# Kernel tuning notes

Measured on AMD Instinct MI355X. Metric: run time of the kernel, lower is better.

Reference implementation:

```python
import jax, jax.numpy as jnp
import numpy as np


def setup_inputs() -> dict:
    key = jax.random.key(0)
    k1, k2, k3, k4 = jax.random.split(key, 4)
    B, N, F, H, C = 16, 4096, 8, 64, 256
    x = jax.random.normal(k1, (B, N, F, H), dtype=jnp.float32)
    W = jax.random.normal(k2, (H, 1), dtype=jnp.float32) / jnp.sqrt(jnp.float32(H))
    b = jax.random.normal(k3, (1,), dtype=jnp.float32) * 0.01
    segment_ids = jax.random.randint(k4, (N,), 0, C)
    return {"x": x, "W": W, "b": b, "segment_ids": segment_ids, "num_coarse": C}


def reference(x, W, b, segment_ids, num_coarse):
    # x: [B, N, F, H]; segment_ids: [N] -> coarse index; output: [B, C, F, H]
    B, N, Fdim, H = x.shape
    seg = segment_ids
    # node scores: Linear(hidden_dim, 1) on mean over feature axis -> [B, N]
    scores = (jnp.einsum('bnfh,ho->bn', x, W) / jnp.float32(Fdim)) + b[0]
    # numerically-stable per-segment softmax over fine nodes within each coarse group
    seg_max = jax.vmap(lambda s: jax.ops.segment_max(s, seg, num_segments=num_coarse))(scores)  # [B, C]
    e = jnp.exp(scores - seg_max[:, seg])                                                        # [B, N]
    denom = jax.vmap(lambda ee: jax.ops.segment_sum(ee, seg, num_segments=num_coarse))(e)        # [B, C]
    w = e / denom[:, seg]                                                                        # [B, N]
    # score-weighted segmented sum of fine features into coarse nodes
    pooled = jax.vmap(
        lambda wb, xb: jax.ops.segment_sum(wb[:, None, None] * xb, seg, num_segments=num_coarse)
    )(w, x)  # [B, C, F, H]
    return pooled
```

## Files before the change

### kernel.cpp

```cpp
#include <hip/hip_runtime.h>

#define B_ 16
#define N_ 4096
#define F_ 8
#define H_ 64
#define C_ 256
#define FH 512
#define CAP 256

__global__ __launch_bounds__(128) void fused_pool_kernel(
    const float* __restrict__ x, const float* __restrict__ W,
    const float* __restrict__ bias, const int* __restrict__ seg,
    float* __restrict__ out)
{
    int b    = blockIdx.x >> 8;
    int c    = blockIdx.x & (C_ - 1);
    int t    = threadIdx.x;
    int wave = t >> 6;
    int lane = t & 63;

    __shared__ int   list[CAP];
    __shared__ int   cnt;
    __shared__ float combine[FH];
    __shared__ float esum_s;

    if (t == 0) cnt = 0;
    __syncthreads();

    const int4* seg4 = (const int4*)seg;
#pragma unroll
    for (int k = 0; k < N_ / (128 * 4); k++) {
        int i4 = t + k * 128;
        int4 s4 = seg4[i4];
        int n0 = i4 * 4;
        if (s4.x == c) { int p = atomicAdd(&cnt, 1); if (p < CAP) list[p] = n0; }
        if (s4.y == c) { int p = atomicAdd(&cnt, 1); if (p < CAP) list[p] = n0 + 1; }
        if (s4.z == c) { int p = atomicAdd(&cnt, 1); if (p < CAP) list[p] = n0 + 2; }
        if (s4.w == c) { int p = atomicAdd(&cnt, 1); if (p < CAP) list[p] = n0 + 3; }
    }
    __syncthreads();
    int m = cnt;
    if (m > CAP) m = CAP;

    float4 w4 = *(const float4*)(W + ((4 * lane) & 63));
    float  bb = bias[0];

    const float4* x4 = (const float4*)x;
    float4 acc0 = {0, 0, 0, 0}, acc1 = {0, 0, 0, 0};
    float  esum = 0.0f;

    for (int i = wave; i < m; i += 2) {
        int n = list[i];
        size_t rb = ((size_t)(b * N_ + n)) * (FH / 4);
        float4 v0 = x4[rb + lane];
        float4 v1 = x4[rb + 64 + lane];
        float p = (v0.x + v1.x) * w4.x + (v0.y + v1.y) * w4.y
                + (v0.z + v1.z) * w4.z + (v0.w + v1.w) * w4.w;
#pragma unroll
        for (int off = 32; off > 0; off >>= 1)
            p += __shfl_xor(p, off, 64);
        float e = __expf(p * (1.0f / F_) + bb);
        esum += e;
        acc0.x += e * v0.x; acc0.y += e * v0.y; acc0.z += e * v0.z; acc0.w += e * v0.w;
        acc1.x += e * v1.x; acc1.y += e * v1.y; acc1.z += e * v1.z; acc1.w += e * v1.w;
    }

    if (wave == 0) {
        *(float4*)&combine[4 * lane]       = acc0;
        *(float4*)&combine[4 * lane + 256] = acc1;
        if (lane == 0) esum_s = esum;
    }
    __syncthreads();
    if (wave == 1) {
        float4 o0 = *(float4*)&combine[4 * lane];
        float4 o1 = *(float4*)&combine[4 * lane + 256];
        float denom = esum + esum_s;
        float inv = (m > 0) ? 1.0f / denom : 0.0f;
        float4 r0, r1;
        r0.x = (acc0.x + o0.x) * inv; r0.y = (acc0.y + o0.y) * inv;
        r0.z = (acc0.z + o0.z) * inv; r0.w = (acc0.w + o0.w) * inv;
        r1.x = (acc1.x + o1.x) * inv; r1.y = (acc1.y + o1.y) * inv;
        r1.z = (acc1.z + o1.z) * inv; r1.w = (acc1.w + o1.w) * inv;
        size_t ob = ((size_t)(b * C_ + c)) * (FH / 4);
        ((float4*)out)[ob + lane]      = r0;
        ((float4*)out)[ob + 64 + lane] = r1;
    }
}

extern "C" void kernel_launch(void* const* d_in, const int* in_sizes, int n_in,
                              void* d_out, int out_size, void* d_ws, size_t ws_size,
                              hipStream_t stream)
{
    const float* x    = (const float*)d_in[0];
    const float* W    = (const float*)d_in[1];
    const float* bias = (const float*)d_in[2];
    const int*   seg  = (const int*)d_in[3];
    float* out = (float*)d_out;

    fused_pool_kernel<<<B_ * C_, 128, 0, stream>>>(x, W, bias, seg, out);
}
```

Measured before the change: 210.4 us.

## Assign one wave per batch, share segment list across four batches per block

Each block now handles one coarse segment for four batches, one wave per batch, so the segment-id scan and list build are amortized over four batches instead of being repeated per batch. Each wave walks the full member list itself and unrolls by two rows for more memory-level parallelism, which removes the cross-wave LDS combine and its barrier. In exchange there are four times fewer blocks and longer serial loops per wave, and register use per thread goes up.

```diff
diff --git a/kernel.cpp b/kernel.cpp
--- a/kernel.cpp
+++ b/kernel.cpp
@@ -8,29 +8,27 @@
 #define FH 512
 #define CAP 256
 
-__global__ __launch_bounds__(128) void fused_pool_kernel(
+__global__ __launch_bounds__(256) void fused_pool_kernel(
     const float* __restrict__ x, const float* __restrict__ W,
     const float* __restrict__ bias, const int* __restrict__ seg,
     float* __restrict__ out)
 {
-    int b    = blockIdx.x >> 8;
     int c    = blockIdx.x & (C_ - 1);
+    int g    = blockIdx.x >> 8;
     int t    = threadIdx.x;
     int wave = t >> 6;
     int lane = t & 63;
+    int b    = g * 4 + wave;
 
-    __shared__ int   list[CAP];
-    __shared__ int   cnt;
-    __shared__ float combine[FH];
-    __shared__ float esum_s;
-
+    __shared__ int list[CAP];
+    __shared__ int cnt;
     if (t == 0) cnt = 0;
     __syncthreads();
 
     const int4* seg4 = (const int4*)seg;
 #pragma unroll
-    for (int k = 0; k < N_ / (128 * 4); k++) {
-        int i4 = t + k * 128;
+    for (int k = 0; k < N_ / (256 * 4); k++) {
+        int i4 = t + k * 256;
         int4 s4 = seg4[i4];
         int n0 = i4 * 4;
         if (s4.x == c) { int p = atomicAdd(&cnt, 1); if (p < CAP) list[p] = n0; }
@@ -46,45 +44,64 @@
     float  bb = bias[0];
 
     const float4* x4 = (const float4*)x;
-    float4 acc0 = {0, 0, 0, 0}, acc1 = {0, 0, 0, 0};
+    size_t batch_base = (size_t)b * N_ * (FH / 4);
+
+    float4 accA0 = {0, 0, 0, 0}, accA1 = {0, 0, 0, 0};
+    float4 accB0 = {0, 0, 0, 0}, accB1 = {0, 0, 0, 0};
     float  esum = 0.0f;
 
-    for (int i = wave; i < m; i += 2) {
-        int n = list[i];
-        size_t rb = ((size_t)(b * N_ + n)) * (FH / 4);
-        float4 v0 = x4[rb + lane];
-        float4 v1 = x4[rb + 64 + lane];
-        float p = (v0.x + v1.x) * w4.x + (v0.y + v1.y) * w4.y
-                + (v0.z + v1.z) * w4.z + (v0.w + v1.w) * w4.w;
+    int i = 0;
+    for (; i + 2 <= m; i += 2) {
+        int na = list[i], nb = list[i + 1];
+        size_t ra = batch_base + (size_t)na * (FH / 4);
+        size_t rb = batch_base + (size_t)nb * (FH / 4);
+        float4 a0 = x4[ra + lane];
+        float4 a1 = x4[ra + 64 + lane];
+        float4 b0 = x4[rb + lane];
+        float4 b1 = x4[rb + 64 + lane];
+
+        float pa = (a0.x + a1.x) * w4.x + (a0.y + a1.y) * w4.y
+                 + (a0.z + a1.z) * w4.z + (a0.w + a1.w) * w4.w;
+        float pb = (b0.x + b1.x) * w4.x + (b0.y + b1.y) * w4.y
+                 + (b0.z + b1.z) * w4.z + (b0.w + b1.w) * w4.w;
+#pragma unroll
+        for (int off = 32; off > 0; off >>= 1) {
+            pa += __shfl_xor(pa, off, 64);
+            pb += __shfl_xor(pb, off, 64);
+        }
+        float ea = __expf(pa * (1.0f / F_) + bb);
+        float eb = __expf(pb * (1.0f / F_) + bb);
+        esum += ea + eb;
+        accA0.x += ea * a0.x; accA0.y += ea * a0.y; accA0.z += ea * a0.z; accA0.w += ea * a0.w;
+        accA1.x += ea * a1.x; accA1.y += ea * a1.y; accA1.z += ea * a1.z; accA1.w += ea * a1.w;
+        accB0.x += eb * b0.x; accB0.y += eb * b0.y; accB0.z += eb * b0.z; accB0.w += eb * b0.w;
+        accB1.x += eb * b1.x; accB1.y += eb * b1.y; accB1.z += eb * b1.z; accB1.w += eb * b1.w;
+    }
+    if (i < m) {
+        int na = list[i];
+        size_t ra = batch_base + (size_t)na * (FH / 4);
+        float4 a0 = x4[ra + lane];
+        float4 a1 = x4[ra + 64 + lane];
+        float pa = (a0.x + a1.x) * w4.x + (a0.y + a1.y) * w4.y
+                 + (a0.z + a1.z) * w4.z + (a0.w + a1.w) * w4.w;
 #pragma unroll
         for (int off = 32; off > 0; off >>= 1)
-            p += __shfl_xor(p, off, 64);
-        float e = __expf(p * (1.0f / F_) + bb);
-        esum += e;
-        acc0.x += e * v0.x; acc0.y += e * v0.y; acc0.z += e * v0.z; acc0.w += e * v0.w;
-        acc1.x += e * v1.x; acc1.y += e * v1.y; acc1.z += e * v1.z; acc1.w += e * v1.w;
+            pa += __shfl_xor(pa, off, 64);
+        float ea = __expf(pa * (1.0f / F_) + bb);
+        esum += ea;
+        accA0.x += ea * a0.x; accA0.y += ea * a0.y; accA0.z += ea * a0.z; accA0.w += ea * a0.w;
+        accA1.x += ea * a1.x; accA1.y += ea * a1.y; accA1.z += ea * a1.z; accA1.w += ea * a1.w;
     }
 
-    if (wave == 0) {
-        *(float4*)&combine[4 * lane]       = acc0;
-        *(float4*)&combine[4 * lane + 256] = acc1;
-        if (lane == 0) esum_s = esum;
-    }
-    __syncthreads();
-    if (wave == 1) {
-        float4 o0 = *(float4*)&combine[4 * lane];
-        float4 o1 = *(float4*)&combine[4 * lane + 256];
-        float denom = esum + esum_s;
-        float inv = (m > 0) ? 1.0f / denom : 0.0f;
-        float4 r0, r1;
-        r0.x = (acc0.x + o0.x) * inv; r0.y = (acc0.y + o0.y) * inv;
-        r0.z = (acc0.z + o0.z) * inv; r0.w = (acc0.w + o0.w) * inv;
-        r1.x = (acc1.x + o1.x) * inv; r1.y = (acc1.y + o1.y) * inv;
-        r1.z = (acc1.z + o1.z) * inv; r1.w = (acc1.w + o1.w) * inv;
-        size_t ob = ((size_t)(b * C_ + c)) * (FH / 4);
-        ((float4*)out)[ob + lane]      = r0;
-        ((float4*)out)[ob + 64 + lane] = r1;
-    }
+    float inv = (m > 0) ? 1.0f / esum : 0.0f;
+    float4 r0, r1;
+    r0.x = (accA0.x + accB0.x) * inv; r0.y = (accA0.y + accB0.y) * inv;
+    r0.z = (accA0.z + accB0.z) * inv; r0.w = (accA0.w + accB0.w) * inv;
+    r1.x = (accA1.x + accB1.x) * inv; r1.y = (accA1.y + accB1.y) * inv;
+    r1.z = (accA1.z + accB1.z) * inv; r1.w = (accA1.w + accB1.w) * inv;
+    size_t ob = ((size_t)(b * C_ + c)) * (FH / 4);
+    ((float4*)out)[ob + lane]      = r0;
+    ((float4*)out)[ob + 64 + lane] = r1;
 }
 
 extern "C" void kernel_launch(void* const* d_in, const int* in_sizes, int n_in,
@@ -97,5 +114,5 @@
     const int*   seg  = (const int*)d_in[3];
     float* out = (float*)d_out;
 
-    fused_pool_kernel<<<B_ * C_, 128, 0, stream>>>(x, W, bias, seg, out);
+    fused_pool_kernel<<<C_ * (B_ / 4), 256, 0, stream>>>(x, W, bias, seg, out);
 }
```

Result: no change. 206.4 us (-1.9%).
